# Kernel tuning notes

Hardware: AMD Instinct MI355X
Metric: run time of the kernel (lower is better)

Reference implementation:

```python
import jax, jax.numpy as jnp
import numpy as np

WINDOW_SIZE = 11
CHANNEL = 3
DATA_RANGE = 1.0
C1 = (0.01 * DATA_RANGE) ** 2
C2 = (0.03 * DATA_RANGE) ** 2


def _gaussian_window(window_size, channel, sigma=1.5):
    coords = np.arange(window_size, dtype=np.float32) - window_size // 2
    g = np.exp(-coords ** 2 / (2 * sigma ** 2))
    g = g / g.sum()
    g2d = g[:, None] * g[None, :]  # [K, K]
    # depthwise conv weight in OIHW with groups=channel -> [C, 1, K, K]
    w = np.broadcast_to(g2d[None, None], (channel, 1, window_size, window_size))
    return jnp.asarray(np.ascontiguousarray(w))


def _dwconv(x, w):
    # depthwise conv, stride 1, SAME padding (== pad window//2 for odd kernel)
    return jax.lax.conv_general_dilated(
        x, w, window_strides=(1, 1), padding='SAME',
        feature_group_count=x.shape[1],
        dimension_numbers=('NCHW', 'OIHW', 'NCHW'))


def setup_inputs() -> dict:
    key = jax.random.key(0)
    k1, k2 = jax.random.split(key)
    img1 = jax.random.normal(k1, (32, 3, 512, 512), dtype=jnp.float32)
    img2 = jax.random.normal(k2, (32, 3, 512, 512), dtype=jnp.float32)
    window = _gaussian_window(WINDOW_SIZE, CHANNEL)
    return {"img1": img1, "img2": img2, "window": window}


def reference(img1, img2, window):
    mu1 = _dwconv(img1, window)
    mu2 = _dwconv(img2, window)
    mu1_sq = mu1 * mu1
    mu2_sq = mu2 * mu2
    mu1_mu2 = mu1 * mu2
    sigma1_sq = jnp.maximum(_dwconv(img1 * img1, window) - mu1_sq, 0.0)
    sigma2_sq = jnp.maximum(_dwconv(img2 * img2, window) - mu2_sq, 0.0)
    sigma12 = _dwconv(img1 * img2, window) - mu1_mu2
    s1 = jnp.sqrt(sigma1_sq)
    s2 = jnp.sqrt(sigma2_sq)
    luminance = (2.0 * mu1_mu2 + C1) / (mu1_sq + mu2_sq + C1)
    contrast = (2.0 * s1 * s2 + C2) / (sigma1_sq + sigma2_sq + C2)
    structure = (sigma12 + C2 / 2) / (s1 * s2 + C2 / 2)
    ssim_map = luminance * contrast * structure
    return jnp.mean(ssim_map)
```

## Files before the change

kernel.cpp:

```cpp
#include <hip/hip_runtime.h>


#define IMG_H 512
#define IMG_W 512
#define N_IMGS 96
#define WAVE_W 64
#define STRIPE 64
#define HALO 5
#define KW 11
#define IN_COLS (WAVE_W + 2*HALO)
#define N_ROWT (IMG_H / STRIPE)
#define N_COLT (IMG_W / WAVE_W)
#define N_BLOCKS (N_IMGS * N_ROWT * N_COLT)
#define T_MAX 77
#define NBINS 256
#define TOTAL_PIX (32.0f * 3.0f * 512.0f * 512.0f)

__global__ __launch_bounds__(64)
__attribute__((amdgpu_waves_per_eu(2, 6)))
void ssim_main(
    const float* __restrict__ img1, const float* __restrict__ img2,
    const float* __restrict__ window, float* __restrict__ bins)
{
    __shared__ float2 ring[KW][IN_COLS];

    const int tid = threadIdx.x;

    float g[KW];
    {
        const float inv = rsqrtf(window[5*KW + 5]);
        #pragma unroll
        for (int k = 0; k < KW; ++k)
            g[k] = __int_as_float(
                __builtin_amdgcn_readfirstlane(
                    __float_as_int(window[5*KW + k] * inv)));
    }

    const int b   = blockIdx.x;
    const int img = b >> 6;
    const int rem = b & 63;
    const int ty  = rem >> 3;
    const int tx  = rem & 7;
    const int r0  = ty * STRIPE;
    const int x0  = tx * WAVE_W;

    const float* __restrict__ p1 = img1 + (size_t)img * (IMG_H * IMG_W);
    const float* __restrict__ p2 = img2 + (size_t)img * (IMG_H * IMG_W);

    const int  gx1  = x0 - HALO + tid;
    const bool c1ok = (unsigned)gx1 < IMG_W;
    const bool tail = tid < (IN_COLS - WAVE_W);
    const int  gx2  = gx1 + WAVE_W;
    const bool c2ok = tail && ((unsigned)gx2 < IMG_W);

    float r_h1[KW], r_h2[KW], r_h11[KW], r_h22[KW], r_h12[KW];
    #pragma unroll
    for (int i = 0; i < KW; ++i) {
        r_h1[i] = 0.f; r_h2[i] = 0.f; r_h11[i] = 0.f; r_h22[i] = 0.f; r_h12[i] = 0.f;
    }

    const float C1 = 1e-4f;
    const float C2 = 9e-4f;
    float sum = 0.f;

    float sa = 0.f, sb = 0.f, sa2 = 0.f, sb2 = 0.f;
    {
        const int gy = r0 - HALO;
        if ((unsigned)gy < IMG_H) {
            const int base = gy * IMG_W;
            if (c1ok) { sa  = p1[base + gx1]; sb  = p2[base + gx1]; }
            if (c2ok) { sa2 = p1[base + gx2]; sb2 = p2[base + gx2]; }
        }
    }

    #pragma unroll 1
    for (int tb = 0; tb < T_MAX; tb += KW) {
        #pragma unroll
        for (int u = 0; u < KW; ++u) {
            const int t = tb + u;

            ring[u][tid] = make_float2(sa, sb);
            if (tail) ring[u][tid + WAVE_W] = make_float2(sa2, sb2);

            __syncthreads();

            {
                const int gy = r0 - HALO + t + 1;
                sa = 0.f; sb = 0.f; sa2 = 0.f; sb2 = 0.f;
                if ((unsigned)gy < IMG_H) {
                    const int base = gy * IMG_W;
                    if (c1ok) { sa  = p1[base + gx1]; sb  = p2[base + gx1]; }
                    if (c2ok) { sa2 = p1[base + gx2]; sb2 = p2[base + gx2]; }
                }
            }

            float h1 = 0.f, h2 = 0.f, h11 = 0.f, h22 = 0.f, h12 = 0.f;
            #pragma unroll
            for (int k = 0; k < KW; ++k) {
                const float2 v = ring[u][tid + k];
                const float t1 = g[k] * v.x;
                const float t2 = g[k] * v.y;
                h1  += t1;
                h2  += t2;
                h11 += t1 * v.x;
                h22 += t2 * v.y;
                h12 += t1 * v.y;
            }
            r_h1[u] = h1; r_h2[u] = h2; r_h11[u] = h11; r_h22[u] = h22; r_h12[u] = h12;

            if (t >= 2*HALO && t < 2*HALO + STRIPE) {
                float mu1 = 0.f, mu2 = 0.f, e11 = 0.f, e22 = 0.f, e12 = 0.f;
                #pragma unroll
                for (int m = 0; m < KW; ++m) {
                    const int slot = (u + 1 + m) % KW;
                    mu1 += g[m] * r_h1[slot];
                    mu2 += g[m] * r_h2[slot];
                    e11 += g[m] * r_h11[slot];
                    e22 += g[m] * r_h22[slot];
                    e12 += g[m] * r_h12[slot];
                }
                const float mu1s = mu1 * mu1, mu2s = mu2 * mu2, mu12 = mu1 * mu2;
                const float s1  = fmaxf(e11 - mu1s, 0.f);
                const float s2  = fmaxf(e22 - mu2s, 0.f);
                const float s12 = e12 - mu12;
                const float num = (2.f * mu12 + C1) * (2.f * s12 + C2);
                const float den = (mu1s + mu2s + C1) * (s1 + s2 + C2);
                sum += num * __builtin_amdgcn_rcpf(den);
            }
        }
    }

    #pragma unroll
    for (int off = 32; off > 0; off >>= 1)
        sum += __shfl_down(sum, off, 64);
    if (tid == 0)
        atomicAdd(&bins[b & (NBINS - 1)], sum);
}

__global__ __launch_bounds__(64) void ssim_final(
    const float* __restrict__ bins, float* __restrict__ out)
{
    const int tid = threadIdx.x;
    float s = 0.f;
    #pragma unroll
    for (int i = 0; i < NBINS / 64; ++i) s += bins[tid + i * 64];
    #pragma unroll
    for (int off = 32; off > 0; off >>= 1)
        s += __shfl_down(s, off, 64);
    if (tid == 0) out[0] = s * (1.0f / TOTAL_PIX);
}

extern "C" void kernel_launch(void* const* d_in, const int* in_sizes, int n_in,
                              void* d_out, int out_size, void* d_ws, size_t ws_size,
                              hipStream_t stream) {
    const float* img1   = (const float*)d_in[0];
    const float* img2   = (const float*)d_in[1];
    const float* window = (const float*)d_in[2];
    float* bins = (float*)d_ws;
    float* out  = (float*)d_out;

    hipMemsetAsync(bins, 0, NBINS * sizeof(float), stream);
    ssim_main<<<N_BLOCKS, 64, 0, stream>>>(img1, img2, window, bins);
    ssim_final<<<1, 64, 0, stream>>>(bins, out);
}
```

Before: 319.7 us.

## Pack four independent stripe waves per block and replace barriers with LDS fences

Each block now holds four waves, each processing its own stripe with a private LDS ring, and the workgroup __syncthreads is replaced by workgroup-scope fences, since every wave only reads its own ring. Boundary loads become clamped-address loads multiplied by masks rather than branches, and the loop trip count is trimmed to 74 with an early break, which removes wasted tail iterations. The aim is to cut barrier cost, per-block launch overhead and divergent load branches. The fence-only sync relies on wave-synchronous behaviour within a single wave for correctness.

```diff
diff --git a/kernel.cpp b/kernel.cpp
--- a/kernel.cpp
+++ b/kernel.cpp
@@ -9,22 +9,26 @@
 #define HALO 5
 #define KW 11
 #define IN_COLS (WAVE_W + 2*HALO)
-#define N_ROWT (IMG_H / STRIPE)
-#define N_COLT (IMG_W / WAVE_W)
-#define N_BLOCKS (N_IMGS * N_ROWT * N_COLT)
-#define T_MAX 77
+#define NWAVES 4
+#define N_STRIPES (N_IMGS * 8 * 8)
+#define N_BLOCKS (N_STRIPES / NWAVES)
+#define T_TOTAL 74
 #define NBINS 256
 #define TOTAL_PIX (32.0f * 3.0f * 512.0f * 512.0f)
 
-__global__ __launch_bounds__(64)
+#define LDS_FENCE() __builtin_amdgcn_fence(__ATOMIC_ACQ_REL, "workgroup")
+
+__global__ __launch_bounds__(64 * NWAVES)
 __attribute__((amdgpu_waves_per_eu(2, 6)))
 void ssim_main(
     const float* __restrict__ img1, const float* __restrict__ img2,
     const float* __restrict__ window, float* __restrict__ bins)
 {
-    __shared__ float2 ring[KW][IN_COLS];
+    __shared__ float2 ring[NWAVES][KW][IN_COLS];
 
-    const int tid = threadIdx.x;
+    const int tid  = threadIdx.x;
+    const int wav  = tid >> 6;
+    const int lane = tid & 63;
 
     float g[KW];
     {
@@ -36,9 +40,9 @@
                     __float_as_int(window[5*KW + k] * inv)));
     }
 
-    const int b   = blockIdx.x;
-    const int img = b >> 6;
-    const int rem = b & 63;
+    const int S   = blockIdx.x * NWAVES + wav;
+    const int img = S >> 6;
+    const int rem = S & 63;
     const int ty  = rem >> 3;
     const int tx  = rem & 7;
     const int r0  = ty * STRIPE;
@@ -47,11 +51,15 @@
     const float* __restrict__ p1 = img1 + (size_t)img * (IMG_H * IMG_W);
     const float* __restrict__ p2 = img2 + (size_t)img * (IMG_H * IMG_W);
 
-    const int  gx1  = x0 - HALO + tid;
-    const bool c1ok = (unsigned)gx1 < IMG_W;
-    const bool tail = tid < (IN_COLS - WAVE_W);
-    const int  gx2  = gx1 + WAVE_W;
-    const bool c2ok = tail && ((unsigned)gx2 < IMG_W);
+    float2 (* __restrict__ wring)[IN_COLS] = ring[wav];
+
+    const int  gx1 = x0 - HALO + lane;
+    const int  gx2 = gx1 + WAVE_W;
+    const int  cx1 = min(max(gx1, 0), IMG_W - 1);
+    const int  cx2 = min(max(gx2, 0), IMG_W - 1);
+    const float cm1 = ((unsigned)gx1 < IMG_W) ? 1.f : 0.f;
+    const float cm2 = ((unsigned)gx2 < IMG_W) ? 1.f : 0.f;
+    const bool tail = lane < (IN_COLS - WAVE_W);
 
     float r_h1[KW], r_h2[KW], r_h11[KW], r_h22[KW], r_h12[KW];
     #pragma unroll
@@ -63,41 +71,45 @@
     const float C2 = 9e-4f;
     float sum = 0.f;
 
-    float sa = 0.f, sb = 0.f, sa2 = 0.f, sb2 = 0.f;
+    float sa, sb, sa2, sb2;
     {
-        const int gy = r0 - HALO;
-        if ((unsigned)gy < IMG_H) {
-            const int base = gy * IMG_W;
-            if (c1ok) { sa  = p1[base + gx1]; sb  = p2[base + gx1]; }
-            if (c2ok) { sa2 = p1[base + gx2]; sb2 = p2[base + gx2]; }
-        }
+        const int gy  = r0 - HALO;
+        const int gyc = min(max(gy, 0), IMG_H - 1);
+        const float rm = ((unsigned)gy < IMG_H) ? 1.f : 0.f;
+        const float* r1 = p1 + gyc * IMG_W;
+        const float* r2 = p2 + gyc * IMG_W;
+        const float m1 = rm * cm1, m2 = rm * cm2;
+        sa  = r1[cx1] * m1;  sb  = r2[cx1] * m1;
+        sa2 = r1[cx2] * m2;  sb2 = r2[cx2] * m2;
     }
 
     #pragma unroll 1
-    for (int tb = 0; tb < T_MAX; tb += KW) {
+    for (int tb = 0; tb < T_TOTAL; tb += KW) {
         #pragma unroll
         for (int u = 0; u < KW; ++u) {
             const int t = tb + u;
+            if (t >= T_TOTAL) break;
 
-            ring[u][tid] = make_float2(sa, sb);
-            if (tail) ring[u][tid + WAVE_W] = make_float2(sa2, sb2);
-
-            __syncthreads();
+            LDS_FENCE();
+            wring[u][lane] = make_float2(sa, sb);
+            if (tail) wring[u][lane + WAVE_W] = make_float2(sa2, sb2);
+            LDS_FENCE();
 
             {
-                const int gy = r0 - HALO + t + 1;
-                sa = 0.f; sb = 0.f; sa2 = 0.f; sb2 = 0.f;
-                if ((unsigned)gy < IMG_H) {
-                    const int base = gy * IMG_W;
-                    if (c1ok) { sa  = p1[base + gx1]; sb  = p2[base + gx1]; }
-                    if (c2ok) { sa2 = p1[base + gx2]; sb2 = p2[base + gx2]; }
-                }
+                const int gy  = r0 - HALO + t + 1;
+                const int gyc = min(max(gy, 0), IMG_H - 1);
+                const float rm = ((unsigned)gy < IMG_H) ? 1.f : 0.f;
+                const float* r1 = p1 + gyc * IMG_W;
+                const float* r2 = p2 + gyc * IMG_W;
+                const float m1 = rm * cm1, m2 = rm * cm2;
+                sa  = r1[cx1] * m1;  sb  = r2[cx1] * m1;
+                sa2 = r1[cx2] * m2;  sb2 = r2[cx2] * m2;
             }
 
             float h1 = 0.f, h2 = 0.f, h11 = 0.f, h22 = 0.f, h12 = 0.f;
             #pragma unroll
             for (int k = 0; k < KW; ++k) {
-                const float2 v = ring[u][tid + k];
+                const float2 v = wring[u][lane + k];
                 const float t1 = g[k] * v.x;
                 const float t2 = g[k] * v.y;
                 h1  += t1;
@@ -108,7 +120,7 @@
             }
             r_h1[u] = h1; r_h2[u] = h2; r_h11[u] = h11; r_h22[u] = h22; r_h12[u] = h12;
 
-            if (t >= 2*HALO && t < 2*HALO + STRIPE) {
+            if (t >= 2*HALO) {
                 float mu1 = 0.f, mu2 = 0.f, e11 = 0.f, e22 = 0.f, e12 = 0.f;
                 #pragma unroll
                 for (int m = 0; m < KW; ++m) {
@@ -133,8 +145,8 @@
     #pragma unroll
     for (int off = 32; off > 0; off >>= 1)
         sum += __shfl_down(sum, off, 64);
-    if (tid == 0)
-        atomicAdd(&bins[b & (NBINS - 1)], sum);
+    if (lane == 0)
+        atomicAdd(&bins[S & (NBINS - 1)], sum);
 }
 
 __global__ __launch_bounds__(64) void ssim_final(
@@ -160,6 +172,6 @@
     float* out  = (float*)d_out;
 
     hipMemsetAsync(bins, 0, NBINS * sizeof(float), stream);
-    ssim_main<<<N_BLOCKS, 64, 0, stream>>>(img1, img2, window, bins);
+    ssim_main<<<N_BLOCKS, 64 * NWAVES, 0, stream>>>(img1, img2, window, bins);
     ssim_final<<<1, 64, 0, stream>>>(bins, out);
 }
```

New measurement: 446.4 us. 1.4x slower.
